# Optimization experiments

Hardware: AMD Instinct MI355X
Metric: run time of the kernel (lower is better)

The kernel has to match this reference:

```python
import jax, jax.numpy as jnp
import numpy as np

B, L, C = 4, 2048, 1024
H = 16
D = C // H
MAX_SCALE_MUL = float(np.log(100.0))


def setup_inputs() -> dict:
    key = jax.random.key(0)
    ks = jax.random.split(key, 4)
    x = jax.random.normal(ks[0], (B, L, C), dtype=jnp.float32)
    attn_bias = jnp.zeros((1, 1, L, L), dtype=jnp.float32)
    qkv_w = jax.random.normal(ks[1], (3 * C, C), dtype=jnp.float32) * (C ** -0.5)
    q_bias = jnp.zeros((C,), dtype=jnp.float32)
    v_bias = jnp.zeros((C,), dtype=jnp.float32)
    scale_mul = jnp.full((1, H, 1, 1), np.log(4.0), dtype=jnp.float32)
    proj_w = jax.random.normal(ks[2], (C, C), dtype=jnp.float32) * (C ** -0.5)
    proj_b = jnp.zeros((C,), dtype=jnp.float32)
    return {"x": x, "attn_bias": attn_bias, "qkv_w": qkv_w, "q_bias": q_bias,
            "v_bias": v_bias, "scale_mul": scale_mul, "proj_w": proj_w, "proj_b": proj_b}


def _l2norm(t, eps=1e-12):
    # matches F.normalize(dim=-1): x / max(||x||, eps)
    n = jnp.sqrt(jnp.sum(t * t, axis=-1, keepdims=True))
    return t / jnp.maximum(n, eps)


def reference(x, attn_bias, qkv_w, q_bias, v_bias, scale_mul, proj_w, proj_b):
    zero_k_bias = jnp.zeros_like(q_bias)
    bias = jnp.concatenate([q_bias, zero_k_bias, v_bias])  # [3C]
    qkv = jnp.einsum('blc,oc->blo', x, qkv_w) + bias        # [B,L,3C]
    qkv = qkv.reshape(B, L, 3, H, D).transpose(2, 0, 3, 1, 4)  # [3,B,H,L,D]
    q, k, v = qkv[0], qkv[1], qkv[2]
    sm = jnp.exp(jnp.minimum(scale_mul, MAX_SCALE_MUL))     # [1,H,1,1]
    q = _l2norm(q) * sm
    k = _l2norm(k)
    scores = jnp.einsum('bhqd,bhkd->bhqk', q, k) * 1.0      # scale=1.0 (l2-norm path)
    scores = scores + attn_bias
    probs = jax.nn.softmax(scores, axis=-1)
    out = jnp.einsum('bhqk,bhkd->bhqd', probs, v)           # [B,H,L,D]
    out = out.transpose(0, 2, 1, 3).reshape(B, L, C)
    return jnp.einsum('blc,oc->blo', out, proj_w) + proj_b
```

## Files before the change

### kernel.cpp

```cpp
#include <hip/hip_runtime.h>
#include <cstdint>


typedef __bf16 bfx8 __attribute__((ext_vector_type(8)));
typedef __bf16 bfx4 __attribute__((ext_vector_type(4)));
typedef float  f32x4 __attribute__((ext_vector_type(4)));
typedef float  f32x16 __attribute__((ext_vector_type(16)));

#define NB   4
#define NH   16
#define SEQ  2048
#define CH   1024
#define DD   64
#define MROWS (NB*SEQ)
#define BHLD  (NB*NH*SEQ*DD)
#define LOG2E 1.44269504088896340736f

__device__ __forceinline__ void async16(void* lds, const void* g) {
  __builtin_amdgcn_global_load_lds((const __attribute__((address_space(1))) void*)g,
                                   (__attribute__((address_space(3))) void*)lds, 16, 0, 0);
}
__device__ __forceinline__ f32x4 mfma16(bfx8 a, bfx8 b, f32x4 c) {
  return __builtin_amdgcn_mfma_f32_16x16x32_bf16(a, b, c, 0, 0, 0);
}
__device__ __forceinline__ f32x16 mfma32(bfx8 a, bfx8 b, f32x16 c) {
  return __builtin_amdgcn_mfma_f32_32x32x16_bf16(a, b, c, 0, 0, 0);
}

extern "C" __device__ float __ocml_exp2_f32(float);
__device__ __forceinline__ float fexp2(float x) {
#if __has_builtin(__builtin_amdgcn_exp2f)
  return __builtin_amdgcn_exp2f(x);
#else
  return __ocml_exp2_f32(x);
#endif
}

__global__ __launch_bounds__(256) void cast_kernel(const float4* __restrict__ src,
                                                   __bf16* __restrict__ dst, int n4) {
  int i = blockIdx.x * 256 + threadIdx.x;
  if (i >= n4) return;
  float4 v = src[i];
  float vv[4] = {v.x, v.y, v.z, v.w};
  bfx4 h;
  #pragma unroll
  for (int j = 0; j < 4; ++j) h[j] = (__bf16)vv[j];
  *(bfx4*)(dst + 4*(size_t)i) = h;
}

__global__ __launch_bounds__(256) void split_kernel(const float4* __restrict__ src,
                                                    __bf16* __restrict__ hi,
                                                    __bf16* __restrict__ lo, int n4) {
  int i = blockIdx.x * 256 + threadIdx.x;
  if (i >= n4) return;
  float4 v = src[i];
  float vv[4] = {v.x, v.y, v.z, v.w};
  bfx4 h, l;
  #pragma unroll
  for (int j = 0; j < 4; ++j) {
    __bf16 hb = (__bf16)vv[j];
    h[j] = hb;
    l[j] = (__bf16)(vv[j] - (float)hb);
  }
  *(bfx4*)(hi + 4*(size_t)i) = h;
  *(bfx4*)(lo + 4*(size_t)i) = l;
}

__global__ __launch_bounds__(256) void scan_nz(const uint4* __restrict__ p, int n4,
                                               int* __restrict__ flag) {
  unsigned acc = 0;
  const int stride = gridDim.x * 256;
  for (int i = blockIdx.x * 256 + threadIdx.x; i < n4; i += stride) {
    uint4 u = p[i];
    acc |= (u.x | u.y | u.z | u.w) & 0x7fffffffu;
  }
  if (acc) atomicOr(flag, 1);
}

__global__ __launch_bounds__(256, 2) void gemmq(
    const __bf16* __restrict__ Ag, const __bf16* __restrict__ Bg,
    const int Ntiles, const int K,
    const float* __restrict__ biasA, const float* __restrict__ biasB,
    const float* __restrict__ scale_mul,
    __bf16* __restrict__ outQ, __bf16* __restrict__ outV)
{
  __shared__ alignas(16) char lds[16384];
  const int tid = threadIdx.x;
  const int lane = tid & 63, w = tid >> 6;
  const int l15 = lane & 15, l4 = lane >> 4;
  const int nwg = (int)gridDim.x;
  const int wk = (int)(blockIdx.x & 7) * (nwg >> 3) + (int)(blockIdx.x >> 3);
  const int mt = wk / Ntiles, nt = wk % Ntiles;
  const int m0 = mt * 128, n0 = nt * 128;
  const int wm = (w >> 1) * 64, wn = (w & 1) * 64;

  const f32x4 zz = {0.f, 0.f, 0.f, 0.f};
  f32x4 acc[4][4];
  #pragma unroll
  for (int a = 0; a < 4; ++a)
    #pragma unroll
    for (int b = 0; b < 4; ++b) acc[a][b] = zz;

  int st_row[2], st_c[2], st_lds[2];
  #pragma unroll
  for (int i = 0; i < 2; ++i) {
    const int s = i*256 + tid;
    st_row[i] = s >> 2;
    st_c[i]   = (s & 3) ^ ((st_row[i] >> 1) & 3);
    st_lds[i] = (i*256 + w*64) * 16;
  }

  for (int k0 = 0; k0 < K; k0 += 32) {
    __syncthreads();
    #pragma unroll
    for (int i = 0; i < 2; ++i) {
      const size_t ga = (size_t)(m0 + st_row[i]) * K + (size_t)(k0 + st_c[i]*8);
      const size_t gb = (size_t)(n0 + st_row[i]) * K + (size_t)(k0 + st_c[i]*8);
      async16(lds +        st_lds[i], Ag + ga);
      async16(lds + 8192 + st_lds[i], Bg + gb);
    }
    __syncthreads();

    bfx8 ah[4], bh[4];
    #pragma unroll
    for (int f = 0; f < 4; ++f) {
      const int ra = wm + f*16 + l15;
      ah[f] = *(const bfx8*)(lds + ra*64 + ((l4 ^ ((ra >> 1) & 3)) * 16));
      const int rb = wn + f*16 + l15;
      bh[f] = *(const bfx8*)(lds + 8192 + rb*64 + ((l4 ^ ((rb >> 1) & 3)) * 16));
    }
    __builtin_amdgcn_s_setprio(1);
    #pragma unroll
    for (int mf = 0; mf < 4; ++mf)
      #pragma unroll
      for (int nf = 0; nf < 4; ++nf)
        acc[mf][nf] = mfma16(ah[mf], bh[nf], acc[mf][nf]);
    __builtin_amdgcn_s_setprio(0);
  }

  const int gcb = n0 + wn;
  const int which = gcb >> 10;
  const int hh = (gcb & (CH-1)) >> 6;
  float smul = 1.f;
  if (which == 0) smul = __expf(fminf(scale_mul[hh], 4.605170185988091f)) * LOG2E;
  #pragma unroll
  for (int mf = 0; mf < 4; ++mf)
    #pragma unroll
    for (int rg = 0; rg < 4; ++rg) {
      #pragma unroll
      for (int nf = 0; nf < 4; ++nf) {
        const int gc = gcb + nf*16 + l15;
        acc[mf][nf][rg] += (which == 0) ? biasA[gc]
                         : ((which == 2) ? biasB[gc - 2*CH] : 0.f);
      }
      const int gr = m0 + wm + mf*16 + 4*l4 + rg;
      const int bb = gr >> 11, ll = gr & (SEQ-1);
      float sc = 1.f;
      if (which < 2) {
        float ss = 0.f;
        #pragma unroll
        for (int nf = 0; nf < 4; ++nf) ss += acc[mf][nf][rg] * acc[mf][nf][rg];
        ss += __shfl_xor(ss, 1); ss += __shfl_xor(ss, 2);
        ss += __shfl_xor(ss, 4); ss += __shfl_xor(ss, 8);
        sc = smul / fmaxf(sqrtf(ss), 1e-12f);
      }
      #pragma unroll
      for (int nf = 0; nf < 4; ++nf) {
        const float v = acc[mf][nf][rg] * sc;
        const int dd = nf*16 + l15;
        if (which < 2)
          outQ[(size_t)which*BHLD + ((size_t)((bb*NH + hh)*SEQ) + ll)*DD + dd] = (__bf16)v;
        else
          outV[((size_t)(bb*NH + hh)*DD + dd)*SEQ + ll] = (__bf16)v;
      }
    }
}

__global__ __launch_bounds__(256, 2) void gemm128s(
    const __bf16* __restrict__ Agh, const __bf16* __restrict__ Agl,
    const __bf16* __restrict__ Bgh, const __bf16* __restrict__ Bgl,
    const int Ntiles, const int K,
    const float* __restrict__ biasA, float* __restrict__ outF)
{
  __shared__ alignas(16) char lds[32768];
  const int tid = threadIdx.x;
  const int lane = tid & 63, w = tid >> 6;
  const int l15 = lane & 15, l4 = lane >> 4;
  const int nwg = (int)gridDim.x;
  const int wk = (int)(blockIdx.x & 7) * (nwg >> 3) + (int)(blockIdx.x >> 3);
  const int mt = wk / Ntiles, nt = wk % Ntiles;
  const int m0 = mt * 128, n0 = nt * 128;
  const int wm = (w >> 1) * 64, wn = (w & 1) * 64;

  const f32x4 zz = {0.f, 0.f, 0.f, 0.f};
  f32x4 acc[4][4];
  #pragma unroll
  for (int a = 0; a < 4; ++a)
    #pragma unroll
    for (int b = 0; b < 4; ++b) acc[a][b] = zz;

  int st_row[2], st_c[2], st_lds[2];
  #pragma unroll
  for (int i = 0; i < 2; ++i) {
    const int s = i*256 + tid;
    st_row[i] = s >> 2;
    st_c[i]   = (s & 3) ^ ((st_row[i] >> 1) & 3);
    st_lds[i] = (i*256 + w*64) * 16;
  }

  for (int k0 = 0; k0 < K; k0 += 32) {
    __syncthreads();
    #pragma unroll
    for (int i = 0; i < 2; ++i) {
      const size_t ga = (size_t)(m0 + st_row[i]) * K + (size_t)(k0 + st_c[i]*8);
      const size_t gb = (size_t)(n0 + st_row[i]) * K + (size_t)(k0 + st_c[i]*8);
      async16(lds +         st_lds[i], Agh + ga);
      async16(lds +  8192 + st_lds[i], Agl + ga);
      async16(lds + 16384 + st_lds[i], Bgh + gb);
      async16(lds + 24576 + st_lds[i], Bgl + gb);
    }
    __syncthreads();

    bfx8 ah[4], al[4], bh[4], bl[4];
    #pragma unroll
    for (int f = 0; f < 4; ++f) {
      const int ra = wm + f*16 + l15;
      const int oa = ra*64 + ((l4 ^ ((ra >> 1) & 3)) * 16);
      ah[f] = *(const bfx8*)(lds + oa);
      al[f] = *(const bfx8*)(lds + 8192 + oa);
      const int rb = wn + f*16 + l15;
      const int ob = rb*64 + ((l4 ^ ((rb >> 1) & 3)) * 16);
      bh[f] = *(const bfx8*)(lds + 16384 + ob);
      bl[f] = *(const bfx8*)(lds + 24576 + ob);
    }
    __builtin_amdgcn_s_setprio(1);
    #pragma unroll
    for (int mf = 0; mf < 4; ++mf)
      #pragma unroll
      for (int nf = 0; nf < 4; ++nf) {
        acc[mf][nf] = mfma16(al[mf], bh[nf], acc[mf][nf]);
        acc[mf][nf] = mfma16(ah[mf], bl[nf], acc[mf][nf]);
        acc[mf][nf] = mfma16(ah[mf], bh[nf], acc[mf][nf]);
      }
    __builtin_amdgcn_s_setprio(0);
  }

  #pragma unroll
  for (int mf = 0; mf < 4; ++mf)
    #pragma unroll
    for (int nf = 0; nf < 4; ++nf)
      #pragma unroll
      for (int rg = 0; rg < 4; ++rg) {
        const int gr = m0 + wm + mf*16 + 4*l4 + rg;
        const int gc = n0 + wn + nf*16 + l15;
        outF[(size_t)gr*CH + gc] = acc[mf][nf][rg] + biasA[gc];
      }
}

__global__ __launch_bounds__(256, 2) void attn_kernel(
    const __bf16* __restrict__ qn, const __bf16* __restrict__ kn,
    const __bf16* __restrict__ vtg, const float* __restrict__ scale_mul,
    const float* __restrict__ bias, const int* __restrict__ flag,
    __bf16* __restrict__ ao_hi, __bf16* __restrict__ ao_lo)
{
  __shared__ alignas(16) char Ks[2][8192];
  __shared__ alignas(16) char Vt[2][8192];

  const int tid = threadIdx.x, lane = tid & 63, w = tid >> 6;
  const int l31 = lane & 31, l5 = lane >> 5;
  const int wk = (int)(blockIdx.x & 7) * 128 + (int)(blockIdx.x >> 3);
  const int qt = wk & 15, h = (wk >> 4) & 15, b = wk >> 8;
  const size_t bh = ((size_t)(b*NH + h)) * SEQ * DD;
  const int hasbias = *flag;

  const float Mh = __expf(fminf(scale_mul[h], 4.605170185988091f)) * LOG2E * 1.01f;

  bfx8 Qf[4];
  const int q0 = qt*128 + w*32;
  #pragma unroll
  for (int kd = 0; kd < 4; ++kd)
    Qf[kd] = *(const bfx8*)(qn + bh + (size_t)(q0 + l31)*DD + kd*16 + l5*8);

  bfx8 ones;
  #pragma unroll
  for (int j = 0; j < 8; ++j) ones[j] = (__bf16)1.0f;

  f32x16 O[2], lsum;
  #pragma unroll
  for (int r = 0; r < 16; ++r) { O[0][r] = 0.f; O[1][r] = 0.f; lsum[r] = 0.f; }
  float m_ = -1e30f, l_ = 0.f;

  auto stage = [&](int t, int buf) {
    const __bf16* ksrc = kn + bh + (size_t)t*64*DD;
    const __bf16* vsrc = vtg + bh + (size_t)t*64;
    #pragma unroll
    for (int i = 0; i < 2; ++i) {
      const int s = i*256 + tid;
      const int row = s >> 3;
      const int c = (s & 7) ^ (row & 7);
      async16(Ks[buf] + (size_t)(i*256 + w*64)*16, ksrc + (size_t)row*DD + c*8);
      async16(Vt[buf] + (size_t)(i*256 + w*64)*16, vsrc + (size_t)row*SEQ + c*8);
    }
  };

  stage(0, 0);
  asm volatile("s_waitcnt vmcnt(0)" ::: "memory");
  __builtin_amdgcn_s_barrier();

  #pragma unroll 1
  for (int t = 0; t < 32; ++t) {
    const int cur = t & 1;
    if (t + 1 < 32) stage(t + 1, cur ^ 1);

    f32x16 ST[2];
    __builtin_amdgcn_s_setprio(1);
    #pragma unroll
    for (int kb = 0; kb < 2; ++kb) {
      f32x16 s;
      #pragma unroll
      for (int r = 0; r < 16; ++r) s[r] = 0.f;
      #pragma unroll
      for (int kd = 0; kd < 4; ++kd) {
        const int row = kb*32 + l31;
        const int c = (2*kd + l5) ^ (l31 & 7);
        const bfx8 Kf = *(const bfx8*)(Ks[cur] + row*128 + c*16);
        s = mfma32(Kf, Qf[kd], s);
      }
      ST[kb] = s;
    }
    __builtin_amdgcn_s_setprio(0);

    unsigned g32[2][4][2];
    if (!hasbias) {
      #pragma unroll
      for (int kb = 0; kb < 2; ++kb)
        #pragma unroll
        for (int rh = 0; rh < 4; ++rh) {
          bfx4 g;
          #pragma unroll
          for (int j = 0; j < 4; ++j)
            g[j] = (__bf16)fexp2(ST[kb][4*rh + j] - Mh);
          union { bfx4 b; unsigned u[2]; } cv; cv.b = g;
          g32[kb][rh][0] = cv.u[0];
          g32[kb][rh][1] = cv.u[1];
        }
    } else {
      const float* bp = bias + (size_t)(q0 + l31)*SEQ + (size_t)t*64;
      float mx = -1e30f;
      #pragma unroll
      for (int kb = 0; kb < 2; ++kb)
        #pragma unroll
        for (int r = 0; r < 16; ++r) {
          ST[kb][r] += bp[32*kb + 4*l5 + (r & 3) + 8*(r >> 2)] * LOG2E;
          mx = fmaxf(mx, ST[kb][r]);
        }
      mx = fmaxf(mx, __shfl_xor(mx, 32));
      const bool skip = __all(mx - m_ <= 12.0f) != 0;
      const float mn = skip ? m_ : fmaxf(m_, mx);
      float rs = 0.f;
      #pragma unroll
      for (int kb = 0; kb < 2; ++kb)
        #pragma unroll
        for (int r = 0; r < 16; ++r) {
          const float pv = fexp2(ST[kb][r] - mn);
          ST[kb][r] = pv;
          rs += pv;
        }
      rs += __shfl_xor(rs, 32);
      if (skip) {
        l_ += rs;
      } else {
        const float corr = fexp2(m_ - mn);
        l_ = l_ * corr + rs;
        m_ = mn;
        #pragma unroll
        for (int db = 0; db < 2; ++db)
          #pragma unroll
          for (int r = 0; r < 16; ++r) O[db][r] *= corr;
      }
      #pragma unroll
      for (int kb = 0; kb < 2; ++kb)
        #pragma unroll
        for (int rh = 0; rh < 4; ++rh) {
          bfx4 g;
          #pragma unroll
          for (int j = 0; j < 4; ++j) g[j] = (__bf16)ST[kb][4*rh + j];
          union { bfx4 b; unsigned u[2]; } cv; cv.b = g;
          g32[kb][rh][0] = cv.u[0];
          g32[kb][rh][1] = cv.u[1];
        }
    }

    bfx8 Pf[4];
    #pragma unroll
    for (int kk = 0; kk < 4; ++kk) {
      const int kb = kk >> 1, e = (kk & 1) * 2;
      unsigned u0 = g32[kb][e][0],   u1 = g32[kb][e][1];
      unsigned v0 = g32[kb][e+1][0], v1 = g32[kb][e+1][1];
      asm volatile("v_permlane32_swap_b32 %0, %1" : "+v"(u0), "+v"(v0));
      asm volatile("v_permlane32_swap_b32 %0, %1" : "+v"(u1), "+v"(v1));
      union { unsigned u[4]; bfx8 bv; } fb;
      fb.u[0] = u0; fb.u[1] = u1; fb.u[2] = v0; fb.u[3] = v1;
      Pf[kk] = fb.bv;
    }

    __builtin_amdgcn_s_setprio(1);
    #pragma unroll
    for (int kk = 0; kk < 4; ++kk) {
      #pragma unroll
      for (int db = 0; db < 2; ++db) {
        const int row = db*32 + l31;
        const int c = (2*kk + l5) ^ (l31 & 7);
        const bfx8 Vf = *(const bfx8*)(Vt[cur] + row*128 + c*16);
        O[db] = mfma32(Vf, Pf[kk], O[db]);
      }
      if (!hasbias) lsum = mfma32(ones, Pf[kk], lsum);
    }
    __builtin_amdgcn_s_setprio(0);

    asm volatile("s_waitcnt vmcnt(0)" ::: "memory");
    __builtin_amdgcn_s_barrier();
  }

  if (!hasbias) l_ = lsum[0];

  const float inv = 1.f / l_;
  const int qg = q0 + l31;
  #pragma unroll
  for (int db = 0; db < 2; ++db)
    #pragma unroll
    for (int rq = 0; rq < 4; ++rq) {
      bfx4 hb, lb;
      #pragma unroll
      for (int j = 0; j < 4; ++j) {
        const float v = O[db][4*rq + j] * inv;
        hb[j] = (__bf16)v;
        lb[j] = (__bf16)(v - (float)hb[j]);
      }
      const size_t idx = ((size_t)(b*SEQ + qg))*CH + h*DD + db*32 + rq*8 + l5*4;
      *(bfx4*)(ao_hi + idx) = hb;
      *(bfx4*)(ao_lo + idx) = lb;
    }
}

extern "C" void kernel_launch(void* const* d_in, const int* in_sizes, int n_in,
                              void* d_out, int out_size, void* d_ws, size_t ws_size,
                              hipStream_t stream) {
  const float* x         = (const float*)d_in[0];
  const float* attn_bias = (const float*)d_in[1];
  const float* qkv_w     = (const float*)d_in[2];
  const float* q_bias    = (const float*)d_in[3];
  const float* v_bias    = (const float*)d_in[4];
  const float* scale_mul = (const float*)d_in[5];
  const float* proj_w    = (const float*)d_in[6];
  const float* proj_b    = (const float*)d_in[7];
  float* out = (float*)d_out;

  char* ws = (char*)d_ws;
  size_t off = 0;
  auto alloc = [&](size_t n) { char* p = ws + off; off += (n + 255) & ~(size_t)255; return p; };
  __bf16* x_h  = (__bf16*)alloc((size_t)MROWS*CH*2);
  __bf16* w_h  = (__bf16*)alloc((size_t)3*CH*CH*2);
  __bf16* p_h  = (__bf16*)alloc((size_t)CH*CH*2);
  __bf16* p_l  = (__bf16*)alloc((size_t)CH*CH*2);
  __bf16* qkvn = (__bf16*)alloc((size_t)2*BHLD*2);
  __bf16* vt   = (__bf16*)alloc((size_t)BHLD*2);
  __bf16* ao_h = (__bf16*)alloc((size_t)MROWS*CH*2);
  __bf16* ao_l = (__bf16*)alloc((size_t)MROWS*CH*2);
  int*    flag = (int*)alloc(256);

  cast_kernel<<<MROWS*CH/4/256, 256, 0, stream>>>((const float4*)x, x_h, MROWS*CH/4);
  cast_kernel<<<3*CH*CH/4/256, 256, 0, stream>>>((const float4*)qkv_w, w_h, 3*CH*CH/4);
  split_kernel<<<CH*CH/4/256, 256, 0, stream>>>((const float4*)proj_w, p_h, p_l, CH*CH/4);

  hipMemsetAsync(flag, 0, sizeof(int), stream);
  scan_nz<<<2048, 256, 0, stream>>>((const uint4*)attn_bias, SEQ*SEQ/4, flag);

  gemmq<<<(MROWS/128)*(3*CH/128), 256, 0, stream>>>(
      x_h, w_h, 3*CH/128, CH, q_bias, v_bias, scale_mul, qkvn, vt);

  attn_kernel<<<NB*NH*(SEQ/128), 256, 0, stream>>>(
      qkvn, qkvn + (size_t)BHLD, vt, scale_mul, attn_bias, flag, ao_h, ao_l);

  gemm128s<<<(MROWS/128)*(CH/128), 256, 0, stream>>>(
      ao_h, ao_l, p_h, p_l, CH/128, CH, proj_b, out);
}
```

Before: 275.1 us.

## Process two 32-row query blocks per wave to reuse K/V fragments

Each wave now handles 64 query rows (two 32-row blocks) instead of 32, so every K and V fragment read from LDS feeds two MFMAs. The attention grid is halved to 256-row query tiles, which halves the K/V global loads per query. The row sum is now accumulated in VALU from the exp values rather than with an extra MFMA against a ones vector. Register pressure roughly doubles for accumulators, and with fewer blocks (512) occupancy and load balance across CUs may suffer.

```diff
diff --git a/kernel.cpp b/kernel.cpp
--- a/kernel.cpp
+++ b/kernel.cpp
@@ -268,27 +268,27 @@
 
   const int tid = threadIdx.x, lane = tid & 63, w = tid >> 6;
   const int l31 = lane & 31, l5 = lane >> 5;
-  const int wk = (int)(blockIdx.x & 7) * 128 + (int)(blockIdx.x >> 3);
-  const int qt = wk & 15, h = (wk >> 4) & 15, b = wk >> 8;
+  const int wk = (int)(blockIdx.x & 7) * 64 + (int)(blockIdx.x >> 3);
+  const int qt = wk & 7, h = (wk >> 3) & 15, b = wk >> 7;
   const size_t bh = ((size_t)(b*NH + h)) * SEQ * DD;
   const int hasbias = *flag;
 
   const float Mh = __expf(fminf(scale_mul[h], 4.605170185988091f)) * LOG2E * 1.01f;
 
-  bfx8 Qf[4];
-  const int q0 = qt*128 + w*32;
-  #pragma unroll
-  for (int kd = 0; kd < 4; ++kd)
-    Qf[kd] = *(const bfx8*)(qn + bh + (size_t)(q0 + l31)*DD + kd*16 + l5*8);
-
-  bfx8 ones;
-  #pragma unroll
-  for (int j = 0; j < 8; ++j) ones[j] = (__bf16)1.0f;
-
-  f32x16 O[2], lsum;
-  #pragma unroll
-  for (int r = 0; r < 16; ++r) { O[0][r] = 0.f; O[1][r] = 0.f; lsum[r] = 0.f; }
-  float m_ = -1e30f, l_ = 0.f;
+  bfx8 Qf[2][4];
+  const int q0 = qt*256 + w*64;
+  #pragma unroll
+  for (int qb = 0; qb < 2; ++qb)
+    #pragma unroll
+    for (int kd = 0; kd < 4; ++kd)
+      Qf[qb][kd] = *(const bfx8*)(qn + bh + (size_t)(q0 + qb*32 + l31)*DD + kd*16 + l5*8);
+
+  f32x16 O[2][2];
+  #pragma unroll
+  for (int qb = 0; qb < 2; ++qb)
+    #pragma unroll
+    for (int r = 0; r < 16; ++r) { O[qb][0][r] = 0.f; O[qb][1][r] = 0.f; }
+  float m_[2] = {-1e30f, -1e30f}, l_[2] = {0.f, 0.f};
 
   auto stage = [&](int t, int buf) {
     const __bf16* ksrc = kn + bh + (size_t)t*64*DD;
@@ -312,135 +312,150 @@
     const int cur = t & 1;
     if (t + 1 < 32) stage(t + 1, cur ^ 1);
 
-    f32x16 ST[2];
+    f32x16 ST[2][2];
+    #pragma unroll
+    for (int qb = 0; qb < 2; ++qb)
+      #pragma unroll
+      for (int kb = 0; kb < 2; ++kb)
+        #pragma unroll
+        for (int r = 0; r < 16; ++r) ST[qb][kb][r] = 0.f;
     __builtin_amdgcn_s_setprio(1);
     #pragma unroll
-    for (int kb = 0; kb < 2; ++kb) {
-      f32x16 s;
-      #pragma unroll
-      for (int r = 0; r < 16; ++r) s[r] = 0.f;
+    for (int kb = 0; kb < 2; ++kb)
       #pragma unroll
       for (int kd = 0; kd < 4; ++kd) {
         const int row = kb*32 + l31;
         const int c = (2*kd + l5) ^ (l31 & 7);
         const bfx8 Kf = *(const bfx8*)(Ks[cur] + row*128 + c*16);
-        s = mfma32(Kf, Qf[kd], s);
-      }
-      ST[kb] = s;
-    }
+        ST[0][kb] = mfma32(Kf, Qf[0][kd], ST[0][kb]);
+        ST[1][kb] = mfma32(Kf, Qf[1][kd], ST[1][kb]);
+      }
     __builtin_amdgcn_s_setprio(0);
 
-    unsigned g32[2][4][2];
+    unsigned g32[2][2][4][2];
     if (!hasbias) {
       #pragma unroll
-      for (int kb = 0; kb < 2; ++kb)
-        #pragma unroll
-        for (int rh = 0; rh < 4; ++rh) {
-          bfx4 g;
+      for (int qb = 0; qb < 2; ++qb) {
+        float ls = 0.f;
+        #pragma unroll
+        for (int kb = 0; kb < 2; ++kb)
           #pragma unroll
-          for (int j = 0; j < 4; ++j)
-            g[j] = (__bf16)fexp2(ST[kb][4*rh + j] - Mh);
-          union { bfx4 b; unsigned u[2]; } cv; cv.b = g;
-          g32[kb][rh][0] = cv.u[0];
-          g32[kb][rh][1] = cv.u[1];
+          for (int rh = 0; rh < 4; ++rh) {
+            bfx4 g;
+            #pragma unroll
+            for (int j = 0; j < 4; ++j) {
+              const float e = fexp2(ST[qb][kb][4*rh + j] - Mh);
+              ls += e;
+              g[j] = (__bf16)e;
+            }
+            union { bfx4 b; unsigned u[2]; } cv; cv.b = g;
+            g32[qb][kb][rh][0] = cv.u[0];
+            g32[qb][kb][rh][1] = cv.u[1];
+          }
+        l_[qb] += ls;
+      }
+    } else {
+      #pragma unroll
+      for (int qb = 0; qb < 2; ++qb) {
+        const float* bp = bias + (size_t)(q0 + qb*32 + l31)*SEQ + (size_t)t*64;
+        float mx = -1e30f;
+        #pragma unroll
+        for (int kb = 0; kb < 2; ++kb)
+          #pragma unroll
+          for (int r = 0; r < 16; ++r) {
+            ST[qb][kb][r] += bp[32*kb + 4*l5 + (r & 3) + 8*(r >> 2)] * LOG2E;
+            mx = fmaxf(mx, ST[qb][kb][r]);
+          }
+        mx = fmaxf(mx, __shfl_xor(mx, 32));
+        const bool skip = __all(mx - m_[qb] <= 12.0f) != 0;
+        const float mn = skip ? m_[qb] : fmaxf(m_[qb], mx);
+        float rs = 0.f;
+        #pragma unroll
+        for (int kb = 0; kb < 2; ++kb)
+          #pragma unroll
+          for (int r = 0; r < 16; ++r) {
+            const float pv = fexp2(ST[qb][kb][r] - mn);
+            ST[qb][kb][r] = pv;
+            rs += pv;
+          }
+        if (skip) {
+          l_[qb] += rs;
+        } else {
+          const float corr = fexp2(m_[qb] - mn);
+          l_[qb] = l_[qb] * corr + rs;
+          m_[qb] = mn;
+          #pragma unroll
+          for (int db = 0; db < 2; ++db)
+            #pragma unroll
+            for (int r = 0; r < 16; ++r) O[qb][db][r] *= corr;
         }
-    } else {
-      const float* bp = bias + (size_t)(q0 + l31)*SEQ + (size_t)t*64;
-      float mx = -1e30f;
-      #pragma unroll
-      for (int kb = 0; kb < 2; ++kb)
-        #pragma unroll
-        for (int r = 0; r < 16; ++r) {
-          ST[kb][r] += bp[32*kb + 4*l5 + (r & 3) + 8*(r >> 2)] * LOG2E;
-          mx = fmaxf(mx, ST[kb][r]);
-        }
-      mx = fmaxf(mx, __shfl_xor(mx, 32));
-      const bool skip = __all(mx - m_ <= 12.0f) != 0;
-      const float mn = skip ? m_ : fmaxf(m_, mx);
-      float rs = 0.f;
-      #pragma unroll
-      for (int kb = 0; kb < 2; ++kb)
-        #pragma unroll
-        for (int r = 0; r < 16; ++r) {
-          const float pv = fexp2(ST[kb][r] - mn);
-          ST[kb][r] = pv;
-          rs += pv;
-        }
-      rs += __shfl_xor(rs, 32);
-      if (skip) {
-        l_ += rs;
-      } else {
-        const float corr = fexp2(m_ - mn);
-        l_ = l_ * corr + rs;
-        m_ = mn;
-        #pragma unroll
-        for (int db = 0; db < 2; ++db)
+        #pragma unroll
+        for (int kb = 0; kb < 2; ++kb)
           #pragma unroll
-          for (int r = 0; r < 16; ++r) O[db][r] *= corr;
-      }
-      #pragma unroll
-      for (int kb = 0; kb < 2; ++kb)
-        #pragma unroll
-        for (int rh = 0; rh < 4; ++rh) {
-          bfx4 g;
-          #pragma unroll
-          for (int j = 0; j < 4; ++j) g[j] = (__bf16)ST[kb][4*rh + j];
-          union { bfx4 b; unsigned u[2]; } cv; cv.b = g;
-          g32[kb][rh][0] = cv.u[0];
-          g32[kb][rh][1] = cv.u[1];
-        }
-    }
-
-    bfx8 Pf[4];
-    #pragma unroll
-    for (int kk = 0; kk < 4; ++kk) {
-      const int kb = kk >> 1, e = (kk & 1) * 2;
-      unsigned u0 = g32[kb][e][0],   u1 = g32[kb][e][1];
-      unsigned v0 = g32[kb][e+1][0], v1 = g32[kb][e+1][1];
-      asm volatile("v_permlane32_swap_b32 %0, %1" : "+v"(u0), "+v"(v0));
-      asm volatile("v_permlane32_swap_b32 %0, %1" : "+v"(u1), "+v"(v1));
-      union { unsigned u[4]; bfx8 bv; } fb;
-      fb.u[0] = u0; fb.u[1] = u1; fb.u[2] = v0; fb.u[3] = v1;
-      Pf[kk] = fb.bv;
-    }
+          for (int rh = 0; rh < 4; ++rh) {
+            bfx4 g;
+            #pragma unroll
+            for (int j = 0; j < 4; ++j) g[j] = (__bf16)ST[qb][kb][4*rh + j];
+            union { bfx4 b; unsigned u[2]; } cv; cv.b = g;
+            g32[qb][kb][rh][0] = cv.u[0];
+            g32[qb][kb][rh][1] = cv.u[1];
+          }
+      }
+    }
+
+    bfx8 Pf[2][4];
+    #pragma unroll
+    for (int qb = 0; qb < 2; ++qb)
+      #pragma unroll
+      for (int kk = 0; kk < 4; ++kk) {
+        const int kb = kk >> 1, e = (kk & 1) * 2;
+        unsigned u0 = g32[qb][kb][e][0],   u1 = g32[qb][kb][e][1];
+        unsigned v0 = g32[qb][kb][e+1][0], v1 = g32[qb][kb][e+1][1];
+        asm volatile("v_permlane32_swap_b32 %0, %1" : "+v"(u0), "+v"(v0));
+        asm volatile("v_permlane32_swap_b32 %0, %1" : "+v"(u1), "+v"(v1));
+        union { unsigned u[4]; bfx8 bv; } fb;
+        fb.u[0] = u0; fb.u[1] = u1; fb.u[2] = v0; fb.u[3] = v1;
+        Pf[qb][kk] = fb.bv;
+      }
 
     __builtin_amdgcn_s_setprio(1);
     #pragma unroll
-    for (int kk = 0; kk < 4; ++kk) {
+    for (int kk = 0; kk < 4; ++kk)
       #pragma unroll
       for (int db = 0; db < 2; ++db) {
         const int row = db*32 + l31;
         const int c = (2*kk + l5) ^ (l31 & 7);
         const bfx8 Vf = *(const bfx8*)(Vt[cur] + row*128 + c*16);
-        O[db] = mfma32(Vf, Pf[kk], O[db]);
-      }
-      if (!hasbias) lsum = mfma32(ones, Pf[kk], lsum);
-    }
+        O[0][db] = mfma32(Vf, Pf[0][kk], O[0][db]);
+        O[1][db] = mfma32(Vf, Pf[1][kk], O[1][db]);
+      }
     __builtin_amdgcn_s_setprio(0);
 
     asm volatile("s_waitcnt vmcnt(0)" ::: "memory");
     __builtin_amdgcn_s_barrier();
   }
 
-  if (!hasbias) l_ = lsum[0];
-
-  const float inv = 1.f / l_;
-  const int qg = q0 + l31;
-  #pragma unroll
-  for (int db = 0; db < 2; ++db)
-    #pragma unroll
-    for (int rq = 0; rq < 4; ++rq) {
-      bfx4 hb, lb;
-      #pragma unroll
-      for (int j = 0; j < 4; ++j) {
-        const float v = O[db][4*rq + j] * inv;
-        hb[j] = (__bf16)v;
-        lb[j] = (__bf16)(v - (float)hb[j]);
-      }
-      const size_t idx = ((size_t)(b*SEQ + qg))*CH + h*DD + db*32 + rq*8 + l5*4;
-      *(bfx4*)(ao_hi + idx) = hb;
-      *(bfx4*)(ao_lo + idx) = lb;
-    }
+  #pragma unroll
+  for (int qb = 0; qb < 2; ++qb) {
+    const float lfull = l_[qb] + __shfl_xor(l_[qb], 32);
+    const float inv = 1.f / lfull;
+    const int qg = q0 + qb*32 + l31;
+    #pragma unroll
+    for (int db = 0; db < 2; ++db)
+      #pragma unroll
+      for (int rq = 0; rq < 4; ++rq) {
+        bfx4 hb, lb;
+        #pragma unroll
+        for (int j = 0; j < 4; ++j) {
+          const float v = O[qb][db][4*rq + j] * inv;
+          hb[j] = (__bf16)v;
+          lb[j] = (__bf16)(v - (float)hb[j]);
+        }
+        const size_t idx = ((size_t)(b*SEQ + qg))*CH + h*DD + db*32 + rq*8 + l5*4;
+        *(bfx4*)(ao_hi + idx) = hb;
+        *(bfx4*)(ao_lo + idx) = lb;
+      }
+  }
 }
 
 extern "C" void kernel_launch(void* const* d_in, const int* in_sizes, int n_in,
@@ -479,7 +494,7 @@
   gemmq<<<(MROWS/128)*(3*CH/128), 256, 0, stream>>>(
       x_h, w_h, 3*CH/128, CH, q_bias, v_bias, scale_mul, qkvn, vt);
 
-  attn_kernel<<<NB*NH*(SEQ/128), 256, 0, stream>>>(
+  attn_kernel<<<NB*NH*(SEQ/256), 256, 0, stream>>>(
       qkvn, qkvn + (size_t)BHLD, vt, scale_mul, attn_bias, flag, ao_h, ao_l);
 
   gemm128s<<<(MROWS/128)*(CH/128), 256, 0, stream>>>(
```

New measurement: 298.9 us. 8.6% more time.
